# Performance work log

Hardware: AMD Instinct MI355X
Metric: run time of the kernel (lower is better)

Reference implementation:

```python
import jax, jax.numpy as jnp
import numpy as np

B, L, D, H, DH = 1, 256, 128, 4, 32  # batch, seq, d_pair, n_head, d_hidden


def setup_inputs() -> dict:
    key = jax.random.key(0)
    ks = jax.random.split(key, 8)
    s = 0.02  # init scale for weights
    return {
        "pair": jax.random.normal(ks[0], (B, L, L, D), jnp.float32),
        "ln_w": jnp.ones((D,), jnp.float32),
        "ln_b": jnp.zeros((D,), jnp.float32),
        "Wq": jax.random.normal(ks[1], (D, H * DH), jnp.float32) * s,
        "Wk": jax.random.normal(ks[2], (D, H * DH), jnp.float32) * s,
        "Wv": jax.random.normal(ks[3], (D, H * DH), jnp.float32) * s,
        "Wb": jax.random.normal(ks[4], (D, H), jnp.float32) * s,
        "Wg": jax.random.normal(ks[5], (D, H * DH), jnp.float32) * s,
        "bg": jnp.ones((H * DH,), jnp.float32),
        "Wo": jax.random.normal(ks[6], (H * DH, D), jnp.float32) * s,
        "bo": jnp.zeros((D,), jnp.float32),
    }


def reference(pair, ln_w, ln_b, Wq, Wk, Wv, Wb, Wg, bg, Wo, bo):
    scale = DH ** -0.5
    # LayerNorm over d_pair
    mu = jnp.mean(pair, axis=-1, keepdims=True)
    var = jnp.mean((pair - mu) ** 2, axis=-1, keepdims=True)
    x = (pair - mu) * jax.lax.rsqrt(var + 1e-5) * ln_w + ln_b
    b, l = x.shape[0], x.shape[1]
    bias = jnp.einsum('bijd,dh->bijh', x, Wb)            # (B, L, L, H)
    gate = jax.nn.sigmoid(x @ Wg + bg)                   # (B, L, L, H*DH)
    q = (x @ Wq).reshape(b, l, l, H, DH) * scale
    k = (x @ Wk).reshape(b, l, l, H, DH)
    v = (x @ Wv).reshape(b, l, l, H, DH)
    # triangle attention over k (third L axis), bias shared across i
    attn = jnp.einsum('bijhd,bikhd->bijkh', q, k) + bias[:, None]
    attn = jax.nn.softmax(attn, axis=3)
    out = jnp.einsum('bijkh,bikhd->bijhd', attn, v).reshape(b, l, l, H * DH)
    out = gate * out
    return out @ Wo + bo
```

## Files before the change

kernel.cpp:

```cpp
#include <hip/hip_runtime.h>
#include <math.h>

#define NPOS 65536

typedef _Float16 f16x8 __attribute__((ext_vector_type(8)));
typedef _Float16 f16x4 __attribute__((ext_vector_type(4)));
typedef float    f32x4 __attribute__((ext_vector_type(4)));

__global__ __launch_bounds__(256) void split_w_kernel(
    const float* __restrict__ Wq, const float* __restrict__ Wk,
    const float* __restrict__ Wv, const float* __restrict__ Wg,
    _Float16* __restrict__ Wt_hi, _Float16* __restrict__ Wt_lo)
{
    int t = blockIdx.x * 256 + threadIdx.x;
    int ng = t >> 7, kk = t & 127;
    int mat = ng >> 7, n = ng & 127;
    const float* W = (mat == 0) ? Wq : (mat == 1) ? Wk : (mat == 2) ? Wv : Wg;
    float x = W[kk * 128 + n];
    _Float16 h = (_Float16)x;
    _Float16 lo = (_Float16)((x - (float)h) * 2048.0f);
    Wt_hi[t] = h;
    Wt_lo[t] = lo;
}

__global__ __launch_bounds__(256, 4) void ln_proj_kernel(
    const float* __restrict__ pair, const float* __restrict__ ln_w, const float* __restrict__ ln_b,
    const float* __restrict__ Wb, const float* __restrict__ bg,
    const _Float16* __restrict__ Wt_hi, const _Float16* __restrict__ Wt_lo,
    float* __restrict__ q, float* __restrict__ k, float* __restrict__ v,
    float* __restrict__ g, float* __restrict__ bias_n)
{
    __shared__ _Float16 xbuf[2][64][136];
    _Float16 (*xh)[136] = xbuf[0];
    _Float16 (*xl)[136] = xbuf[1];

    const int tid = threadIdx.x;
    const int p0  = blockIdx.x * 64;
    const int r   = tid >> 2;
    const int cb  = (tid & 3) * 32;

    float xv[32];
    {
        const float4* pr = (const float4*)(pair + (size_t)(p0 + r) * 128 + cb);
        #pragma unroll
        for (int i = 0; i < 8; ++i) {
            float4 t = pr[i];
            xv[i * 4 + 0] = t.x; xv[i * 4 + 1] = t.y;
            xv[i * 4 + 2] = t.z; xv[i * 4 + 3] = t.w;
        }
    }
    float sum = 0.f, sq = 0.f;
    #pragma unroll
    for (int i = 0; i < 32; ++i) { sum += xv[i]; sq += xv[i] * xv[i]; }
    sum += __shfl_xor(sum, 1); sq += __shfl_xor(sq, 1);
    sum += __shfl_xor(sum, 2); sq += __shfl_xor(sq, 2);
    float mean = sum * (1.f / 128.f);
    float var  = sq * (1.f / 128.f) - mean * mean;
    float rstd = rsqrtf(var + 1e-5f);

    float b0 = 0.f, b1 = 0.f, b2 = 0.f, b3 = 0.f;
    #pragma unroll
    for (int i8 = 0; i8 < 4; ++i8) {
        float4 lw0 = *(const float4*)(ln_w + cb + i8 * 8);
        float4 lw1 = *(const float4*)(ln_w + cb + i8 * 8 + 4);
        float4 lb0 = *(const float4*)(ln_b + cb + i8 * 8);
        float4 lb1 = *(const float4*)(ln_b + cb + i8 * 8 + 4);
        float lw[8] = {lw0.x, lw0.y, lw0.z, lw0.w, lw1.x, lw1.y, lw1.z, lw1.w};
        float lb[8] = {lb0.x, lb0.y, lb0.z, lb0.w, lb1.x, lb1.y, lb1.z, lb1.w};
        f16x8 hv, lv;
        #pragma unroll
        for (int j = 0; j < 8; ++j) {
            int i = i8 * 8 + j;
            float xn = (xv[i] - mean) * rstd * lw[j] + lb[j];
            _Float16 h = (_Float16)xn;
            hv[j] = h;
            lv[j] = (_Float16)((xn - (float)h) * 2048.0f);
            float4 wb = *(const float4*)(Wb + (size_t)(cb + i) * 4);
            b0 = fmaf(xn, wb.x, b0); b1 = fmaf(xn, wb.y, b1);
            b2 = fmaf(xn, wb.z, b2); b3 = fmaf(xn, wb.w, b3);
        }
        *(f16x8*)&xh[r][cb + i8 * 8] = hv;
        *(f16x8*)&xl[r][cb + i8 * 8] = lv;
    }
    b0 += __shfl_xor(b0, 1); b1 += __shfl_xor(b1, 1);
    b2 += __shfl_xor(b2, 1); b3 += __shfl_xor(b3, 1);
    b0 += __shfl_xor(b0, 2); b1 += __shfl_xor(b1, 2);
    b2 += __shfl_xor(b2, 2); b3 += __shfl_xor(b3, 2);
    if ((tid & 3) == 0) {
        int p = p0 + r;
        bias_n[0 * NPOS + p] = b0;
        bias_n[1 * NPOS + p] = b1;
        bias_n[2 * NPOS + p] = b2;
        bias_n[3 * NPOS + p] = b3;
    }
    __syncthreads();

    const int w  = tid >> 6, l = tid & 63;
    const int lm = l & 15, lg = l >> 4;
    const int arow = w * 16 + lm;

    f16x8 ahf[4], alf[4];
    #pragma unroll
    for (int kt = 0; kt < 4; ++kt) {
        ahf[kt] = *(const f16x8*)&xh[arow][kt * 32 + lg * 8];
        alf[kt] = *(const f16x8*)&xl[arow][kt * 32 + lg * 8];
    }

    _Float16 (*Bh)[136] = xbuf[0];
    _Float16 (*Bl)[136] = xbuf[1];
    float* stg = (float*)&xbuf[0][0][0];

    const float scale = 0.17677669529663687f;

    for (int chunk = 0; chunk < 8; ++chunk) {
        const int mat = chunk >> 1;
        const int colhalf = (chunk & 1) * 64;
        float* dst = (mat == 0) ? q : (mat == 1) ? k : (mat == 2) ? v : g;

        __syncthreads();

        {
            const _Float16* srch = Wt_hi + (size_t)(chunk * 64) * 128;
            const _Float16* srcl = Wt_lo + (size_t)(chunk * 64) * 128;
            #pragma unroll
            for (int it = 0; it < 4; ++it) {
                int idx = it * 256 + tid;
                int row = idx >> 4, kc8 = (idx & 15) * 8;
                *(f16x8*)&Bh[row][kc8] = *(const f16x8*)(srch + row * 128 + kc8);
                *(f16x8*)&Bl[row][kc8] = *(const f16x8*)(srcl + row * 128 + kc8);
            }
        }
        __syncthreads();

        f32x4 acch[4], accc[4];
        #pragma unroll
        for (int ct = 0; ct < 4; ++ct) {
            acch[ct] = (f32x4){0.f, 0.f, 0.f, 0.f};
            accc[ct] = (f32x4){0.f, 0.f, 0.f, 0.f};
        }
        #pragma unroll
        for (int kt = 0; kt < 4; ++kt) {
            const int koff = kt * 32 + lg * 8;
            #pragma unroll
            for (int ct = 0; ct < 4; ++ct) {
                f16x8 bh = *(const f16x8*)&Bh[ct * 16 + lm][koff];
                f16x8 bl = *(const f16x8*)&Bl[ct * 16 + lm][koff];
                acch[ct] = __builtin_amdgcn_mfma_f32_16x16x32_f16(ahf[kt], bh, acch[ct], 0, 0, 0);
                accc[ct] = __builtin_amdgcn_mfma_f32_16x16x32_f16(alf[kt], bh, accc[ct], 0, 0, 0);
                accc[ct] = __builtin_amdgcn_mfma_f32_16x16x32_f16(ahf[kt], bl, accc[ct], 0, 0, 0);
            }
        }

        __syncthreads();

        #pragma unroll
        for (int ct = 0; ct < 4; ++ct) {
            const int col = ct * 16 + lm;
            float bgv = (mat == 3) ? bg[colhalf + col] : 0.f;
            #pragma unroll
            for (int rr = 0; rr < 4; ++rr) {
                float val = acch[ct][rr] + accc[ct][rr] * (1.0f / 2048.0f);
                if (mat == 0) val *= scale;
                if (mat == 3) val = 1.f / (1.f + __expf(-(val + bgv)));
                stg[(w * 16 + lg * 4 + rr) * 68 + col] = val;
            }
        }
        __syncthreads();

        #pragma unroll
        for (int it = 0; it < 4; ++it) {
            int idx = it * 256 + tid;
            int row = idx >> 4, c4 = (idx & 15) * 4;
            float4 val = *(const float4*)&stg[row * 68 + c4];
            *(float4*)(dst + (size_t)(p0 + row) * 128 + colhalf + c4) = val;
        }
    }
}

__global__ __launch_bounds__(256, 2) void attn_kernel(
    const float* __restrict__ q, const float* __restrict__ k, const float* __restrict__ v,
    const float* __restrict__ g, const float* __restrict__ bias_n, float* __restrict__ go)
{
    __shared__ _Float16 Khs[32][48];
    __shared__ _Float16 Kls[32][48];
    __shared__ _Float16 Vts[32][48];
    __shared__ float    Pb[4][64][36];

    const int tid  = threadIdx.x;
    const int w    = tid >> 6;
    const int lane = tid & 63;
    const int lg   = lane >> 4, lm = lane & 15;
    const int i = blockIdx.x >> 2, h = blockIdx.x & 3;
    const size_t base = (size_t)i * 256 * 128 + (size_t)h * 32;
    const int j0w = w * 64;

    f16x8 qh[4], ql[4];
    #pragma unroll
    for (int jt = 0; jt < 4; ++jt) {
        const float* qp = q + base + (size_t)(j0w + jt * 16 + lm) * 128 + lg * 8;
        float4 a = *(const float4*)qp;
        float4 b = *(const float4*)(qp + 4);
        float qv[8] = {a.x, a.y, a.z, a.w, b.x, b.y, b.z, b.w};
        #pragma unroll
        for (int e = 0; e < 8; ++e) {
            _Float16 hh = (_Float16)qv[e];
            qh[jt][e] = hh;
            ql[jt][e] = (_Float16)((qv[e] - (float)hh) * 2048.0f);
        }
    }

    float Oacc[4][2][4] = {};
    float mrow[4][4], lrow[4][4];
    #pragma unroll
    for (int jt = 0; jt < 4; ++jt)
        #pragma unroll
        for (int rr = 0; rr < 4; ++rr) { mrow[jt][rr] = -1e30f; lrow[jt][rr] = 0.f; }

    for (int kc = 0; kc < 256; kc += 32) {
        __syncthreads();
        {
            int r  = tid >> 3;
            int c0 = (tid & 7) * 4;
            float4 kv4 = *(const float4*)(k + base + (size_t)(kc + r) * 128 + c0);
            float kvv[4] = {kv4.x, kv4.y, kv4.z, kv4.w};
            f16x4 h4, l4;
            #pragma unroll
            for (int e = 0; e < 4; ++e) {
                _Float16 hh = (_Float16)kvv[e];
                h4[e] = hh;
                l4[e] = (_Float16)((kvv[e] - (float)hh) * 2048.0f);
            }
            *(f16x4*)&Khs[r][c0] = h4;
            *(f16x4*)&Kls[r][c0] = l4;
            float4 vv4 = *(const float4*)(v + base + (size_t)(kc + r) * 128 + c0);
            Vts[c0 + 0][r] = (_Float16)vv4.x;
            Vts[c0 + 1][r] = (_Float16)vv4.y;
            Vts[c0 + 2][r] = (_Float16)vv4.z;
            Vts[c0 + 3][r] = (_Float16)vv4.w;
        }
        __syncthreads();

        f16x8 bh[2], bl[2], vf[2];
        #pragma unroll
        for (int kt = 0; kt < 2; ++kt) {
            bh[kt] = *(const f16x8*)&Khs[kt * 16 + lm][lg * 8];
            bl[kt] = *(const f16x8*)&Kls[kt * 16 + lm][lg * 8];
            vf[kt] = *(const f16x8*)&Vts[kt * 16 + lm][lg * 8];
        }

        float Sv[4][2][4];
        #pragma unroll
        for (int jt = 0; jt < 4; ++jt) {
            #pragma unroll
            for (int kt = 0; kt < 2; ++kt) {
                const float* bj = bias_n + (size_t)h * NPOS
                                + (size_t)(j0w + jt * 16 + lg * 4) * 256 + kc + kt * 16 + lm;
                f32x4 chi = {bj[0], bj[256], bj[512], bj[768]};
                f32x4 ccr = {0.f, 0.f, 0.f, 0.f};
                chi = __builtin_amdgcn_mfma_f32_16x16x32_f16(qh[jt], bh[kt], chi, 0, 0, 0);
                ccr = __builtin_amdgcn_mfma_f32_16x16x32_f16(ql[jt], bh[kt], ccr, 0, 0, 0);
                ccr = __builtin_amdgcn_mfma_f32_16x16x32_f16(qh[jt], bl[kt], ccr, 0, 0, 0);
                #pragma unroll
                for (int rr = 0; rr < 4; ++rr)
                    Sv[jt][kt][rr] = chi[rr] + ccr[rr] * (1.0f / 2048.0f);
            }
        }

        #pragma unroll
        for (int jt = 0; jt < 4; ++jt) {
            #pragma unroll
            for (int rr = 0; rr < 4; ++rr) {
                float s0 = Sv[jt][0][rr], s1 = Sv[jt][1][rr];
                float mx = fmaxf(s0, s1);
                mx = fmaxf(mx, __shfl_xor(mx, 1));
                mx = fmaxf(mx, __shfl_xor(mx, 2));
                mx = fmaxf(mx, __shfl_xor(mx, 4));
                mx = fmaxf(mx, __shfl_xor(mx, 8));
                float mo = mrow[jt][rr];
                float mn = fmaxf(mo, mx);
                float alpha = __expf(mo - mn);
                mrow[jt][rr] = mn;
                float p0 = __expf(s0 - mn);
                float p1 = __expf(s1 - mn);
                float ps = p0 + p1;
                ps += __shfl_xor(ps, 1);
                ps += __shfl_xor(ps, 2);
                ps += __shfl_xor(ps, 4);
                ps += __shfl_xor(ps, 8);
                lrow[jt][rr] = lrow[jt][rr] * alpha + ps;
                Oacc[jt][0][rr] *= alpha;
                Oacc[jt][1][rr] *= alpha;
                int row = jt * 16 + lg * 4 + rr;
                Pb[w][row][lm]      = p0;
                Pb[w][row][16 + lm] = p1;
            }
        }

        #pragma unroll
        for (int jt = 0; jt < 4; ++jt) {
            f32x4 pa = *(const f32x4*)&Pb[w][jt * 16 + lm][lg * 8];
            f32x4 pb2 = *(const f32x4*)&Pb[w][jt * 16 + lm][lg * 8 + 4];
            f16x8 pf;
            #pragma unroll
            for (int e = 0; e < 4; ++e) {
                pf[e]     = (_Float16)pa[e];
                pf[e + 4] = (_Float16)pb2[e];
            }
            #pragma unroll
            for (int dt = 0; dt < 2; ++dt) {
                f32x4 c = {Oacc[jt][dt][0], Oacc[jt][dt][1], Oacc[jt][dt][2], Oacc[jt][dt][3]};
                c = __builtin_amdgcn_mfma_f32_16x16x32_f16(pf, vf[dt], c, 0, 0, 0);
                Oacc[jt][dt][0] = c[0]; Oacc[jt][dt][1] = c[1];
                Oacc[jt][dt][2] = c[2]; Oacc[jt][dt][3] = c[3];
            }
        }
    }

    #pragma unroll
    for (int jt = 0; jt < 4; ++jt) {
        #pragma unroll
        for (int rr = 0; rr < 4; ++rr) {
            int j = j0w + jt * 16 + lg * 4 + rr;
            float inv = 1.0f / lrow[jt][rr];
            #pragma unroll
            for (int dt = 0; dt < 2; ++dt) {
                int col = dt * 16 + lm;
                float val = Oacc[jt][dt][rr] * inv;
                float gv = g[base + (size_t)j * 128 + col];
                go[base + (size_t)j * 128 + col] = val * gv;
            }
        }
    }
}

__global__ __launch_bounds__(256) void out_proj_kernel(
    const float* __restrict__ go, const float* __restrict__ Wo, const float* __restrict__ bo,
    float* __restrict__ out)
{
    __shared__ float at[64][140];
    const int tid = threadIdx.x;
    const int p0  = blockIdx.x * 64;

    for (int i = tid; i < 64 * 32; i += 256) {
        int row = i >> 5, c4 = (i & 31) * 4;
        float4 val = *(const float4*)(go + (size_t)(p0 + row) * 128 + c4);
        at[row][c4 + 0] = val.x; at[row][c4 + 1] = val.y;
        at[row][c4 + 2] = val.z; at[row][c4 + 3] = val.w;
    }
    __syncthreads();

    const int ty = tid >> 4, tx = tid & 15;
    float acc[4][8] = {};
    #pragma unroll 2
    for (int kk = 0; kk < 128; ++kk) {
        float4 wA = *(const float4*)(Wo + kk * 128 + tx * 8);
        float4 wB = *(const float4*)(Wo + kk * 128 + tx * 8 + 4);
        #pragma unroll
        for (int rr = 0; rr < 4; ++rr) {
            float av = at[ty * 4 + rr][kk];
            acc[rr][0] = fmaf(av, wA.x, acc[rr][0]);
            acc[rr][1] = fmaf(av, wA.y, acc[rr][1]);
            acc[rr][2] = fmaf(av, wA.z, acc[rr][2]);
            acc[rr][3] = fmaf(av, wA.w, acc[rr][3]);
            acc[rr][4] = fmaf(av, wB.x, acc[rr][4]);
            acc[rr][5] = fmaf(av, wB.y, acc[rr][5]);
            acc[rr][6] = fmaf(av, wB.z, acc[rr][6]);
            acc[rr][7] = fmaf(av, wB.w, acc[rr][7]);
        }
    }
    #pragma unroll
    for (int rr = 0; rr < 4; ++rr) {
        float ov[8];
        #pragma unroll
        for (int c = 0; c < 8; ++c) ov[c] = acc[rr][c] + bo[tx * 8 + c];
        float* outp = out + (size_t)(p0 + ty * 4 + rr) * 128 + tx * 8;
        *(float4*)outp       = *(float4*)ov;
        *(float4*)(outp + 4) = *(float4*)(ov + 4);
    }
}

extern "C" void kernel_launch(void* const* d_in, const int* in_sizes, int n_in,
                              void* d_out, int out_size, void* d_ws, size_t ws_size,
                              hipStream_t stream) {
    const float* pair = (const float*)d_in[0];
    const float* ln_w = (const float*)d_in[1];
    const float* ln_b = (const float*)d_in[2];
    const float* Wq   = (const float*)d_in[3];
    const float* Wk   = (const float*)d_in[4];
    const float* Wv   = (const float*)d_in[5];
    const float* Wb   = (const float*)d_in[6];
    const float* Wg   = (const float*)d_in[7];
    const float* bg   = (const float*)d_in[8];
    const float* Wo   = (const float*)d_in[9];
    const float* bo   = (const float*)d_in[10];

    float* ws     = (float*)d_ws;
    float* q      = ws;
    float* k      = ws + (size_t)1 * NPOS * 128;
    float* v      = ws + (size_t)2 * NPOS * 128;
    float* g      = ws + (size_t)3 * NPOS * 128;
    float* go     = ws + (size_t)4 * NPOS * 128;
    float* bias_n = ws + (size_t)5 * NPOS * 128;
    float* out    = (float*)d_out;

    _Float16* Wt_hi = (_Float16*)d_out;
    _Float16* Wt_lo = Wt_hi + (size_t)512 * 128;

    hipLaunchKernelGGL(split_w_kernel, dim3(256), dim3(256), 0, stream,
                       Wq, Wk, Wv, Wg, Wt_hi, Wt_lo);
    hipLaunchKernelGGL(ln_proj_kernel, dim3(1024), dim3(256), 0, stream,
                       pair, ln_w, ln_b, Wb, bg, Wt_hi, Wt_lo, q, k, v, g, bias_n);
    hipLaunchKernelGGL(attn_kernel, dim3(1024), dim3(256), 0, stream,
                       q, k, v, g, bias_n, go);
    hipLaunchKernelGGL(out_proj_kernel, dim3(1024), dim3(256), 0, stream,
                       go, Wo, bo, out);
}
```

Before: 283.6 us.

## Transpose attention MFMA operands, prefetch K/V, store probabilities as fp16

Swaps the MFMA operand order so each lane holds a full query row's scores. This turns the softmax row reductions from 4-step shuffles per row into in-register max/sum plus two cross-group shuffles, and lets bias, gate and output accesses use float4 vectors. It also stores probabilities to shared memory as fp16 instead of fp32, register-prefetches the next K/V chunk across the barrier, pads the LDS arrays differently, and raises launch bounds to 3 blocks per CU. The cost is higher register pressure from the prefetch against a tighter occupancy target, which could cause spills.

New measurement: 264.0 us. -6.9%, faster.

```diff
diff --git a/kernel.cpp b/kernel.cpp
--- a/kernel.cpp
+++ b/kernel.cpp
@@ -177,14 +177,14 @@
     }
 }
 
-__global__ __launch_bounds__(256, 2) void attn_kernel(
+__global__ __launch_bounds__(256, 3) void attn_kernel(
     const float* __restrict__ q, const float* __restrict__ k, const float* __restrict__ v,
     const float* __restrict__ g, const float* __restrict__ bias_n, float* __restrict__ go)
 {
-    __shared__ _Float16 Khs[32][48];
-    __shared__ _Float16 Kls[32][48];
-    __shared__ _Float16 Vts[32][48];
-    __shared__ float    Pb[4][64][36];
+    __shared__ _Float16 Khs[32][56];
+    __shared__ _Float16 Kls[32][56];
+    __shared__ _Float16 Vts[32][56];
+    __shared__ _Float16 Pb[4][64][40];
 
     const int tid  = threadIdx.x;
     const int w    = tid >> 6;
@@ -209,20 +209,21 @@
         }
     }
 
-    float Oacc[4][2][4] = {};
-    float mrow[4][4], lrow[4][4];
-    #pragma unroll
-    for (int jt = 0; jt < 4; ++jt)
-        #pragma unroll
-        for (int rr = 0; rr < 4; ++rr) { mrow[jt][rr] = -1e30f; lrow[jt][rr] = 0.f; }
+    float Oacc[2][4][4] = {};
+    float mrow[4], lrow[4];
+    #pragma unroll
+    for (int jt = 0; jt < 4; ++jt) { mrow[jt] = -1e30f; lrow[jt] = 0.f; }
+
+    const int sr  = tid >> 3;
+    const int sc0 = (tid & 7) * 4;
+
+    float4 kpre = *(const float4*)(k + base + (size_t)sr * 128 + sc0);
+    float4 vpre = *(const float4*)(v + base + (size_t)sr * 128 + sc0);
 
     for (int kc = 0; kc < 256; kc += 32) {
         __syncthreads();
         {
-            int r  = tid >> 3;
-            int c0 = (tid & 7) * 4;
-            float4 kv4 = *(const float4*)(k + base + (size_t)(kc + r) * 128 + c0);
-            float kvv[4] = {kv4.x, kv4.y, kv4.z, kv4.w};
+            float kvv[4] = {kpre.x, kpre.y, kpre.z, kpre.w};
             f16x4 h4, l4;
             #pragma unroll
             for (int e = 0; e < 4; ++e) {
@@ -230,15 +231,18 @@
                 h4[e] = hh;
                 l4[e] = (_Float16)((kvv[e] - (float)hh) * 2048.0f);
             }
-            *(f16x4*)&Khs[r][c0] = h4;
-            *(f16x4*)&Kls[r][c0] = l4;
-            float4 vv4 = *(const float4*)(v + base + (size_t)(kc + r) * 128 + c0);
-            Vts[c0 + 0][r] = (_Float16)vv4.x;
-            Vts[c0 + 1][r] = (_Float16)vv4.y;
-            Vts[c0 + 2][r] = (_Float16)vv4.z;
-            Vts[c0 + 3][r] = (_Float16)vv4.w;
-        }
-        __syncthreads();
+            *(f16x4*)&Khs[sr][sc0] = h4;
+            *(f16x4*)&Kls[sr][sc0] = l4;
+            Vts[sc0 + 0][sr] = (_Float16)vpre.x;
+            Vts[sc0 + 1][sr] = (_Float16)vpre.y;
+            Vts[sc0 + 2][sr] = (_Float16)vpre.z;
+            Vts[sc0 + 3][sr] = (_Float16)vpre.w;
+        }
+        __syncthreads();
+        if (kc + 32 < 256) {
+            kpre = *(const float4*)(k + base + (size_t)(kc + 32 + sr) * 128 + sc0);
+            vpre = *(const float4*)(v + base + (size_t)(kc + 32 + sr) * 128 + sc0);
+        }
 
         f16x8 bh[2], bl[2], vf[2];
         #pragma unroll
@@ -248,87 +252,80 @@
             vf[kt] = *(const f16x8*)&Vts[kt * 16 + lm][lg * 8];
         }
 
-        float Sv[4][2][4];
         #pragma unroll
         for (int jt = 0; jt < 4; ++jt) {
-            #pragma unroll
-            for (int kt = 0; kt < 2; ++kt) {
-                const float* bj = bias_n + (size_t)h * NPOS
-                                + (size_t)(j0w + jt * 16 + lg * 4) * 256 + kc + kt * 16 + lm;
-                f32x4 chi = {bj[0], bj[256], bj[512], bj[768]};
-                f32x4 ccr = {0.f, 0.f, 0.f, 0.f};
-                chi = __builtin_amdgcn_mfma_f32_16x16x32_f16(qh[jt], bh[kt], chi, 0, 0, 0);
-                ccr = __builtin_amdgcn_mfma_f32_16x16x32_f16(ql[jt], bh[kt], ccr, 0, 0, 0);
-                ccr = __builtin_amdgcn_mfma_f32_16x16x32_f16(qh[jt], bl[kt], ccr, 0, 0, 0);
+            const float* bj = bias_n + (size_t)h * NPOS
+                            + (size_t)(j0w + jt * 16 + lm) * 256 + kc + lg * 4;
+            float4 b0 = *(const float4*)bj;
+            float4 b1 = *(const float4*)(bj + 16);
+            f32x4 c0h = {b0.x, b0.y, b0.z, b0.w};
+            f32x4 c1h = {b1.x, b1.y, b1.z, b1.w};
+            f32x4 c0l = {0.f, 0.f, 0.f, 0.f}, c1l = {0.f, 0.f, 0.f, 0.f};
+            c0h = __builtin_amdgcn_mfma_f32_16x16x32_f16(bh[0], qh[jt], c0h, 0, 0, 0);
+            c0l = __builtin_amdgcn_mfma_f32_16x16x32_f16(bl[0], qh[jt], c0l, 0, 0, 0);
+            c0l = __builtin_amdgcn_mfma_f32_16x16x32_f16(bh[0], ql[jt], c0l, 0, 0, 0);
+            c1h = __builtin_amdgcn_mfma_f32_16x16x32_f16(bh[1], qh[jt], c1h, 0, 0, 0);
+            c1l = __builtin_amdgcn_mfma_f32_16x16x32_f16(bl[1], qh[jt], c1l, 0, 0, 0);
+            c1l = __builtin_amdgcn_mfma_f32_16x16x32_f16(bh[1], ql[jt], c1l, 0, 0, 0);
+
+            float s[8];
+            #pragma unroll
+            for (int rr = 0; rr < 4; ++rr) {
+                s[rr]     = c0h[rr] + c0l[rr] * (1.0f / 2048.0f);
+                s[4 + rr] = c1h[rr] + c1l[rr] * (1.0f / 2048.0f);
+            }
+            float mx = s[0];
+            #pragma unroll
+            for (int e = 1; e < 8; ++e) mx = fmaxf(mx, s[e]);
+            mx = fmaxf(mx, __shfl_xor(mx, 16));
+            mx = fmaxf(mx, __shfl_xor(mx, 32));
+            float mn = fmaxf(mrow[jt], mx);
+            float alpha = __expf(mrow[jt] - mn);
+            mrow[jt] = mn;
+            float p[8], ps = 0.f;
+            #pragma unroll
+            for (int e = 0; e < 8; ++e) { p[e] = __expf(s[e] - mn); ps += p[e]; }
+            ps += __shfl_xor(ps, 16);
+            ps += __shfl_xor(ps, 32);
+            lrow[jt] = lrow[jt] * alpha + ps;
+            #pragma unroll
+            for (int dt = 0; dt < 2; ++dt)
                 #pragma unroll
-                for (int rr = 0; rr < 4; ++rr)
-                    Sv[jt][kt][rr] = chi[rr] + ccr[rr] * (1.0f / 2048.0f);
-            }
+                for (int rr = 0; rr < 4; ++rr) Oacc[dt][jt][rr] *= alpha;
+            f16x4 pa, pbv;
+            #pragma unroll
+            for (int rr = 0; rr < 4; ++rr) { pa[rr] = (_Float16)p[rr]; pbv[rr] = (_Float16)p[4 + rr]; }
+            *(f16x4*)&Pb[w][jt * 16 + lm][lg * 4]      = pa;
+            *(f16x4*)&Pb[w][jt * 16 + lm][16 + lg * 4] = pbv;
         }
 
         #pragma unroll
         for (int jt = 0; jt < 4; ++jt) {
-            #pragma unroll
-            for (int rr = 0; rr < 4; ++rr) {
-                float s0 = Sv[jt][0][rr], s1 = Sv[jt][1][rr];
-                float mx = fmaxf(s0, s1);
-                mx = fmaxf(mx, __shfl_xor(mx, 1));
-                mx = fmaxf(mx, __shfl_xor(mx, 2));
-                mx = fmaxf(mx, __shfl_xor(mx, 4));
-                mx = fmaxf(mx, __shfl_xor(mx, 8));
-                float mo = mrow[jt][rr];
-                float mn = fmaxf(mo, mx);
-                float alpha = __expf(mo - mn);
-                mrow[jt][rr] = mn;
-                float p0 = __expf(s0 - mn);
-                float p1 = __expf(s1 - mn);
-                float ps = p0 + p1;
-                ps += __shfl_xor(ps, 1);
-                ps += __shfl_xor(ps, 2);
-                ps += __shfl_xor(ps, 4);
-                ps += __shfl_xor(ps, 8);
-                lrow[jt][rr] = lrow[jt][rr] * alpha + ps;
-                Oacc[jt][0][rr] *= alpha;
-                Oacc[jt][1][rr] *= alpha;
-                int row = jt * 16 + lg * 4 + rr;
-                Pb[w][row][lm]      = p0;
-                Pb[w][row][16 + lm] = p1;
-            }
-        }
-
-        #pragma unroll
-        for (int jt = 0; jt < 4; ++jt) {
-            f32x4 pa = *(const f32x4*)&Pb[w][jt * 16 + lm][lg * 8];
-            f32x4 pb2 = *(const f32x4*)&Pb[w][jt * 16 + lm][lg * 8 + 4];
-            f16x8 pf;
-            #pragma unroll
-            for (int e = 0; e < 4; ++e) {
-                pf[e]     = (_Float16)pa[e];
-                pf[e + 4] = (_Float16)pb2[e];
-            }
+            f16x8 pf = *(const f16x8*)&Pb[w][jt * 16 + lm][lg * 8];
             #pragma unroll
             for (int dt = 0; dt < 2; ++dt) {
-                f32x4 c = {Oacc[jt][dt][0], Oacc[jt][dt][1], Oacc[jt][dt][2], Oacc[jt][dt][3]};
-                c = __builtin_amdgcn_mfma_f32_16x16x32_f16(pf, vf[dt], c, 0, 0, 0);
-                Oacc[jt][dt][0] = c[0]; Oacc[jt][dt][1] = c[1];
-                Oacc[jt][dt][2] = c[2]; Oacc[jt][dt][3] = c[3];
+                f32x4 c = {Oacc[dt][jt][0], Oacc[dt][jt][1], Oacc[dt][jt][2], Oacc[dt][jt][3]};
+                c = __builtin_amdgcn_mfma_f32_16x16x32_f16(vf[dt], pf, c, 0, 0, 0);
+                Oacc[dt][jt][0] = c[0]; Oacc[dt][jt][1] = c[1];
+                Oacc[dt][jt][2] = c[2]; Oacc[dt][jt][3] = c[3];
             }
         }
     }
 
     #pragma unroll
     for (int jt = 0; jt < 4; ++jt) {
-        #pragma unroll
-        for (int rr = 0; rr < 4; ++rr) {
-            int j = j0w + jt * 16 + lg * 4 + rr;
-            float inv = 1.0f / lrow[jt][rr];
-            #pragma unroll
-            for (int dt = 0; dt < 2; ++dt) {
-                int col = dt * 16 + lm;
-                float val = Oacc[jt][dt][rr] * inv;
-                float gv = g[base + (size_t)j * 128 + col];
-                go[base + (size_t)j * 128 + col] = val * gv;
-            }
+        const int j = j0w + jt * 16 + lm;
+        const float inv = 1.0f / lrow[jt];
+        #pragma unroll
+        for (int dt = 0; dt < 2; ++dt) {
+            const float* gp = g + base + (size_t)j * 128 + dt * 16 + lg * 4;
+            float4 gv = *(const float4*)gp;
+            float4 ov;
+            ov.x = Oacc[dt][jt][0] * inv * gv.x;
+            ov.y = Oacc[dt][jt][1] * inv * gv.y;
+            ov.z = Oacc[dt][jt][2] * inv * gv.z;
+            ov.w = Oacc[dt][jt][3] * inv * gv.w;
+            *(float4*)(go + base + (size_t)j * 128 + dt * 16 + lg * 4) = ov;
         }
     }
 }
```
